# Performance work log

Hardware: AMD Instinct MI355X
Metric: run time of the kernel (lower is better)

## Reference

```python
import jax, jax.numpy as jnp
import numpy as np

N = 500000   # number of points
C = 64       # in_channels == out_channels
L = 4        # n_layers


def setup_inputs() -> dict:
    key = jax.random.key(0)
    ks = jax.random.split(key, 7)
    s = np.float32(1.0 / np.sqrt(C))  # keep activations O(1) across layers
    return {
        "features": jax.random.normal(ks[0], (N, C), jnp.float32),
        "points": jax.random.normal(ks[1], (N, 3), jnp.float32),
        "nuv": jax.random.normal(ks[2], (N, 3, 3), jnp.float32),
        "W0": jax.random.normal(ks[3], (L, C, C), jnp.float32) * s,  # linear_transform
        "b0": jnp.zeros((L, C), jnp.float32),
        "W1": jax.random.normal(ks[4], (L, C, C), jnp.float32) * s,  # linear_block[0]
        "b1": jnp.zeros((L, C), jnp.float32),
        "W2": jax.random.normal(ks[5], (L, C, C), jnp.float32) * s,  # linear_block[2]
        "b2": jnp.zeros((L, C), jnp.float32),
    }


def reference(features, points, nuv, W0, b0, W1, b1, W2, b2):
    # Faithful to the torch source: inside each DMaSIFConvBlock the dmasif_conv
    # output is overwritten by linear_transform(features), so the effective math
    # per block is: x = Linear2(relu(Linear1(Linear0(x)))).
    # points / nuv / ranges do not influence the output.
    del points, nuv

    def step(x, params):
        w0, c0, w1, c1, w2, c2 = params
        h = x @ w0 + c0                      # linear_transform
        h = jax.nn.relu(h @ w1 + c1)          # linear_block: Linear + ReLU
        h = h @ w2 + c2                      # linear_block: Linear
        return h, None

    out, _ = jax.lax.scan(step, features, (W0, b0, W1, b1, W2, b2))
    return out
```

## Files before the change

### kernel.cpp

```cpp
#include <hip/hip_runtime.h>
#include <stdint.h>

#define CH 64
#define NPTS 500000
#define NTILE (NPTS / 32)
#define NSTEP 12
#define BLK 256
#define WPB (BLK / 64)

typedef float floatx16 __attribute__((ext_vector_type(16)));
typedef __bf16 bf16x8 __attribute__((ext_vector_type(8)));

__device__ __forceinline__ unsigned pk(float odd, float even) {
    return __builtin_amdgcn_perm(__float_as_uint(odd), __float_as_uint(even), 0x07060302u);
}
__device__ __forceinline__ float hif(float x) {
    return __uint_as_float(__float_as_uint(x) & 0xffff0000u);
}

struct U16 { unsigned a, b, c, d; };
__device__ __forceinline__ bf16x8 asb4(unsigned x0, unsigned x1, unsigned x2, unsigned x3) {
    U16 t{x0, x1, x2, x3};
    return __builtin_bit_cast(bf16x8, t);
}
__device__ __forceinline__ bf16x8 asbu4(uint4 v) {
    return __builtin_bit_cast(bf16x8, v);
}

typedef __attribute__((address_space(3))) void lds_void;
typedef const __attribute__((address_space(1))) void gm_void;
__device__ __forceinline__ void gload_lds16(const void* g, void* l) {
    __builtin_amdgcn_global_load_lds((gm_void*)g, (lds_void*)l, 16, 0, 0);
}

__global__ void prep_weights(const float* __restrict__ W0,
                             const float* __restrict__ W1,
                             const float* __restrict__ W2,
                             uint4* __restrict__ wsA) {
    const int g  = blockIdx.x * blockDim.x + threadIdx.x;
    const int mp = g & 31;
    const int h  = (g >> 5) & 1;
    const int q  = (g >> 6) & 3;
    const int mt = (g >> 8) & 1;
    const int pl = (g >> 9) & 1;
    const int s  = g >> 10;
    const float* Wb = (s % 3 == 0) ? W0 : ((s % 3 == 1) ? W1 : W2);
    const float* Ws = Wb + (s / 3) * CH * CH;
    const int m   = mt * 32 + mp;
    const int col = (m & ~12) | ((m & 4) << 1) | ((m & 8) >> 1);
    unsigned o[4];
    #pragma unroll
    for (int d = 0; d < 4; ++d) {
        float e = Ws[(16 * q + 8 * h + 2 * d) * CH + col];
        float v = Ws[(16 * q + 8 * h + 2 * d + 1) * CH + col];
        if (pl) { e = e - hif(e); v = v - hif(v); }
        o[d] = pk(v, e);
    }
    wsA[g] = make_uint4(o[0], o[1], o[2], o[3]);
}

__global__ __launch_bounds__(BLK, 4) void mlp12_mfma(
    const float* __restrict__ feat,
    const uint4* __restrict__ wsA,
    const float* __restrict__ b0,
    const float* __restrict__ b1,
    const float* __restrict__ b2,
    float* __restrict__ out)
{
    __shared__ uint4 sA[2][1024];

    const int tid  = threadIdx.x;
    const int lane = tid & 63;
    const int wv   = tid >> 6;
    int wid = blockIdx.x * WPB + wv;
    if (wid > NTILE - 1) wid = NTILE - 1;
    const int n = lane & 31;
    const int h = lane >> 5;
    const size_t row = (size_t)(wid * 32 + n) * CH;

    float4 fa[4], fb[4];
    {
        const float* frow = feat + row + 8 * h;
        #pragma unroll
        for (int q = 0; q < 4; ++q) {
            fa[q] = *(const float4*)(frow + 16 * q);
            fb[q] = *(const float4*)(frow + 16 * q + 4);
        }
    }

    {
        const char* g = (const char*)wsA;
        #pragma unroll
        for (int c = 0; c < 4; ++c)
            gload_lds16(g + (wv * 4 + c) * 1024 + lane * 16,
                        (char*)&sA[0][0] + (wv * 4 + c) * 1024);
    }
    __syncthreads();

    unsigned Bhi[4][4], Blo[4][4];
    floatx16 acc0, acc1;

    #pragma unroll
    for (int s = 0; s < NSTEP; ++s) {
        const int b = s & 1;

        if (s + 1 < NSTEP) {
            const char* g = (const char*)wsA + (size_t)(s + 1) * 16384;
            #pragma unroll
            for (int c = 0; c < 4; ++c)
                gload_lds16(g + (wv * 4 + c) * 1024 + lane * 16,
                            (char*)&sA[1 - b][0] + (wv * 4 + c) * 1024);
        }

        const uint4* base = &sA[b][0];

        uint4 Acur[4], Anx[4];
        #pragma unroll
        for (int t = 0; t < 4; ++t) Acur[t] = base[(t * 4 + 0) * 64 + lane];

        if (s == 0) {
            #pragma unroll
            for (int q = 0; q < 4; ++q) {
                float e0 = fa[q].x, o0 = fa[q].y, e1 = fa[q].z, o1 = fa[q].w;
                float e2 = fb[q].x, o2 = fb[q].y, e3 = fb[q].z, o3 = fb[q].w;
                Bhi[q][0] = pk(o0, e0); Bhi[q][1] = pk(o1, e1);
                Bhi[q][2] = pk(o2, e2); Bhi[q][3] = pk(o3, e3);
                Blo[q][0] = pk(o0 - hif(o0), e0 - hif(e0));
                Blo[q][1] = pk(o1 - hif(o1), e1 - hif(e1));
                Blo[q][2] = pk(o2 - hif(o2), e2 - hif(e2));
                Blo[q][3] = pk(o3 - hif(o3), e3 - hif(e3));
            }
        } else {
            const bool relu = (s % 3 == 2);
            #pragma unroll
            for (int q = 0; q < 4; ++q) {
                const int rr = q & 1;
                #pragma unroll
                for (int d = 0; d < 4; ++d) {
                    float e, o;
                    if (q < 2) { e = acc0[8 * rr + 2 * d]; o = acc0[8 * rr + 2 * d + 1]; }
                    else       { e = acc1[8 * rr + 2 * d]; o = acc1[8 * rr + 2 * d + 1]; }
                    if (relu) { e = fmaxf(e, 0.f); o = fmaxf(o, 0.f); }
                    Bhi[q][d] = pk(o, e);
                    Blo[q][d] = pk(o - hif(o), e - hif(e));
                }
            }
        }

        {
            const float* bs = ((s % 3 == 0) ? b0 : (s % 3 == 1) ? b1 : b2) + (s / 3) * CH;
            #pragma unroll
            for (int rq = 0; rq < 4; ++rq) {
                const int off = 16 * (rq >> 1) + 8 * h + 4 * (rq & 1);
                float4 v0 = *(const float4*)(bs + off);
                float4 v1 = *(const float4*)(bs + 32 + off);
                acc0[4 * rq + 0] = v0.x; acc0[4 * rq + 1] = v0.y;
                acc0[4 * rq + 2] = v0.z; acc0[4 * rq + 3] = v0.w;
                acc1[4 * rq + 0] = v1.x; acc1[4 * rq + 1] = v1.y;
                acc1[4 * rq + 2] = v1.z; acc1[4 * rq + 3] = v1.w;
            }
        }

        #pragma unroll
        for (int q = 0; q < 4; ++q) {
            if (q < 3) {
                #pragma unroll
                for (int t = 0; t < 4; ++t) Anx[t] = base[(t * 4 + q + 1) * 64 + lane];
            }
            bf16x8 bh = asb4(Bhi[q][0], Bhi[q][1], Bhi[q][2], Bhi[q][3]);
            bf16x8 bl = asb4(Blo[q][0], Blo[q][1], Blo[q][2], Blo[q][3]);
            acc0 = __builtin_amdgcn_mfma_f32_32x32x16_bf16(asbu4(Acur[0]), bh, acc0, 0, 0, 0);
            acc1 = __builtin_amdgcn_mfma_f32_32x32x16_bf16(asbu4(Acur[1]), bh, acc1, 0, 0, 0);
            acc0 = __builtin_amdgcn_mfma_f32_32x32x16_bf16(asbu4(Acur[2]), bh, acc0, 0, 0, 0);
            acc1 = __builtin_amdgcn_mfma_f32_32x32x16_bf16(asbu4(Acur[3]), bh, acc1, 0, 0, 0);
            acc0 = __builtin_amdgcn_mfma_f32_32x32x16_bf16(asbu4(Acur[0]), bl, acc0, 0, 0, 0);
            acc1 = __builtin_amdgcn_mfma_f32_32x32x16_bf16(asbu4(Acur[1]), bl, acc1, 0, 0, 0);
            #pragma unroll
            for (int t = 0; t < 4; ++t) Acur[t] = Anx[t];
        }

        __syncthreads();
    }

    float* orow = out + row;
    #pragma unroll
    for (int rq = 0; rq < 4; ++rq) {
        float4 v0, v1;
        v0.x = acc0[4 * rq + 0]; v0.y = acc0[4 * rq + 1];
        v0.z = acc0[4 * rq + 2]; v0.w = acc0[4 * rq + 3];
        v1.x = acc1[4 * rq + 0]; v1.y = acc1[4 * rq + 1];
        v1.z = acc1[4 * rq + 2]; v1.w = acc1[4 * rq + 3];
        const int off = 16 * (rq >> 1) + 8 * h + 4 * (rq & 1);
        *(float4*)(orow + off)      = v0;
        *(float4*)(orow + 32 + off) = v1;
    }
}

extern "C" void kernel_launch(void* const* d_in, const int* in_sizes, int n_in,
                              void* d_out, int out_size, void* d_ws, size_t ws_size,
                              hipStream_t stream) {
    const float* feat = (const float*)d_in[0];
    const float* W0 = (const float*)d_in[3];
    const float* b0 = (const float*)d_in[4];
    const float* W1 = (const float*)d_in[5];
    const float* b1 = (const float*)d_in[6];
    const float* W2 = (const float*)d_in[7];
    const float* b2 = (const float*)d_in[8];
    float* out = (float*)d_out;
    uint4* wsA = (uint4*)d_ws;

    prep_weights<<<48, 256, 0, stream>>>(W0, W1, W2, wsA);

    const int grid = (NTILE + WPB - 1) / WPB;
    mlp12_mfma<<<grid, BLK, 0, stream>>>(feat, wsA, b0, b1, b2, out);
}
```

Measured before the change: 330.7 us.

## Process two 32-row tiles per wave to reuse LDS weight fragments

Each wave now computes 64 points as two independent 32-row tiles, sharing each weight fragment loaded from LDS across both tiles' MFMAs. This halves LDS weight reads and per-wave bias/setup overhead per point, and gives the MFMA pipe more independent accumulators to interleave. The 12 steps are split into two non-unrolled passes of six to bound code size. The extra accumulators and B fragments raise register pressure, so the occupancy hint drops from 4 to 3 blocks. The last wave handles its odd tile by duplicating rows.

```diff
diff --git a/kernel.cpp b/kernel.cpp
--- a/kernel.cpp
+++ b/kernel.cpp
@@ -3,7 +3,7 @@
 
 #define CH 64
 #define NPTS 500000
-#define NTILE (NPTS / 32)
+#define NW 7813
 #define NSTEP 12
 #define BLK 256
 #define WPB (BLK / 64)
@@ -32,6 +32,8 @@
 __device__ __forceinline__ void gload_lds16(const void* g, void* l) {
     __builtin_amdgcn_global_load_lds((gm_void*)g, (lds_void*)l, 16, 0, 0);
 }
+
+#define MFMA_B(A, Bv, C) __builtin_amdgcn_mfma_f32_32x32x16_bf16(asbu4(A), Bv, C, 0, 0, 0)
 
 __global__ void prep_weights(const float* __restrict__ W0,
                              const float* __restrict__ W1,
@@ -59,7 +61,7 @@
     wsA[g] = make_uint4(o[0], o[1], o[2], o[3]);
 }
 
-__global__ __launch_bounds__(BLK, 4) void mlp12_mfma(
+__global__ __launch_bounds__(BLK, 3) void mlp12_mfma(
     const float* __restrict__ feat,
     const uint4* __restrict__ wsA,
     const float* __restrict__ b0,
@@ -73,20 +75,11 @@
     const int lane = tid & 63;
     const int wv   = tid >> 6;
     int wid = blockIdx.x * WPB + wv;
-    if (wid > NTILE - 1) wid = NTILE - 1;
+    if (wid > NW - 1) wid = NW - 1;
     const int n = lane & 31;
     const int h = lane >> 5;
-    const size_t row = (size_t)(wid * 32 + n) * CH;
-
-    float4 fa[4], fb[4];
-    {
-        const float* frow = feat + row + 8 * h;
-        #pragma unroll
-        for (int q = 0; q < 4; ++q) {
-            fa[q] = *(const float4*)(frow + 16 * q);
-            fb[q] = *(const float4*)(frow + 16 * q + 4);
-        }
-    }
+    const size_t row0 = ((size_t)wid * 64 + n) * CH;
+    const size_t row1 = (wid == NW - 1) ? row0 : row0 + (size_t)32 * CH;
 
     {
         const char* g = (const char*)wsA;
@@ -95,104 +88,153 @@
             gload_lds16(g + (wv * 4 + c) * 1024 + lane * 16,
                         (char*)&sA[0][0] + (wv * 4 + c) * 1024);
     }
+
+    unsigned Bhi[2][4][4], Blo[2][4][4];
+    {
+        const float* f0 = feat + row0 + 8 * h;
+        const float* f1 = feat + row1 + 8 * h;
+        #pragma unroll
+        for (int q = 0; q < 4; ++q) {
+            float4 va = *(const float4*)(f0 + 16 * q);
+            float4 vb = *(const float4*)(f0 + 16 * q + 4);
+            Bhi[0][q][0] = pk(va.y, va.x);  Bhi[0][q][1] = pk(va.w, va.z);
+            Bhi[0][q][2] = pk(vb.y, vb.x);  Bhi[0][q][3] = pk(vb.w, vb.z);
+            Blo[0][q][0] = pk(va.y - hif(va.y), va.x - hif(va.x));
+            Blo[0][q][1] = pk(va.w - hif(va.w), va.z - hif(va.z));
+            Blo[0][q][2] = pk(vb.y - hif(vb.y), vb.x - hif(vb.x));
+            Blo[0][q][3] = pk(vb.w - hif(vb.w), vb.z - hif(vb.z));
+            float4 vc = *(const float4*)(f1 + 16 * q);
+            float4 vd = *(const float4*)(f1 + 16 * q + 4);
+            Bhi[1][q][0] = pk(vc.y, vc.x);  Bhi[1][q][1] = pk(vc.w, vc.z);
+            Bhi[1][q][2] = pk(vd.y, vd.x);  Bhi[1][q][3] = pk(vd.w, vd.z);
+            Blo[1][q][0] = pk(vc.y - hif(vc.y), vc.x - hif(vc.x));
+            Blo[1][q][1] = pk(vc.w - hif(vc.w), vc.z - hif(vc.z));
+            Blo[1][q][2] = pk(vd.y - hif(vd.y), vd.x - hif(vd.x));
+            Blo[1][q][3] = pk(vd.w - hif(vd.w), vd.z - hif(vd.z));
+        }
+    }
     __syncthreads();
 
-    unsigned Bhi[4][4], Blo[4][4];
-    floatx16 acc0, acc1;
-
-    #pragma unroll
-    for (int s = 0; s < NSTEP; ++s) {
-        const int b = s & 1;
-
-        if (s + 1 < NSTEP) {
-            const char* g = (const char*)wsA + (size_t)(s + 1) * 16384;
+    floatx16 ac00, ac01, ac10, ac11;
+
+    #pragma unroll 1
+    for (int k = 0; k < 2; ++k) {
+        const char*  gk  = (const char*)wsA + (size_t)k * 6 * 16384;
+        const float* bb0 = b0 + 2 * k * CH;
+        const float* bb1 = b1 + 2 * k * CH;
+        const float* bb2 = b2 + 2 * k * CH;
+        #pragma unroll
+        for (int j = 0; j < 6; ++j) {
+            const int s = 6 * k + j;
+            const int b = j & 1;
+
+            if (s + 1 < NSTEP) {
+                const char* g = gk + (size_t)(j + 1) * 16384;
+                #pragma unroll
+                for (int c = 0; c < 4; ++c)
+                    gload_lds16(g + (wv * 4 + c) * 1024 + lane * 16,
+                                (char*)&sA[1 - b][0] + (wv * 4 + c) * 1024);
+            }
+
+            const uint4* base = &sA[b][0];
+
+            uint4 Acur[4], Anx[4];
             #pragma unroll
-            for (int c = 0; c < 4; ++c)
-                gload_lds16(g + (wv * 4 + c) * 1024 + lane * 16,
-                            (char*)&sA[1 - b][0] + (wv * 4 + c) * 1024);
-        }
-
-        const uint4* base = &sA[b][0];
-
-        uint4 Acur[4], Anx[4];
-        #pragma unroll
-        for (int t = 0; t < 4; ++t) Acur[t] = base[(t * 4 + 0) * 64 + lane];
-
-        if (s == 0) {
+            for (int t = 0; t < 4; ++t) Acur[t] = base[(t * 4 + 0) * 64 + lane];
+
+            if (s > 0) {
+                const bool relu = (j % 3 == 2);
+                #pragma unroll
+                for (int q = 0; q < 4; ++q) {
+                    const int rr = q & 1;
+                    #pragma unroll
+                    for (int d = 0; d < 4; ++d) {
+                        float e, o;
+                        if (q < 2) { e = ac00[8*rr+2*d]; o = ac00[8*rr+2*d+1]; }
+                        else       { e = ac01[8*rr+2*d]; o = ac01[8*rr+2*d+1]; }
+                        if (relu) { e = fmaxf(e, 0.f); o = fmaxf(o, 0.f); }
+                        Bhi[0][q][d] = pk(o, e);
+                        Blo[0][q][d] = pk(o - hif(o), e - hif(e));
+                    }
+                }
+                #pragma unroll
+                for (int q = 0; q < 4; ++q) {
+                    const int rr = q & 1;
+                    #pragma unroll
+                    for (int d = 0; d < 4; ++d) {
+                        float e, o;
+                        if (q < 2) { e = ac10[8*rr+2*d]; o = ac10[8*rr+2*d+1]; }
+                        else       { e = ac11[8*rr+2*d]; o = ac11[8*rr+2*d+1]; }
+                        if (relu) { e = fmaxf(e, 0.f); o = fmaxf(o, 0.f); }
+                        Bhi[1][q][d] = pk(o, e);
+                        Blo[1][q][d] = pk(o - hif(o), e - hif(e));
+                    }
+                }
+            }
+
+            {
+                const float* bs = ((j % 3 == 0) ? bb0 : (j % 3 == 1) ? bb1 : bb2)
+                                  + (j / 3) * CH;
+                #pragma unroll
+                for (int rq = 0; rq < 4; ++rq) {
+                    const int off = 16 * (rq >> 1) + 8 * h + 4 * (rq & 1);
+                    float4 v0 = *(const float4*)(bs + off);
+                    float4 v1 = *(const float4*)(bs + 32 + off);
+                    ac00[4*rq+0] = v0.x; ac00[4*rq+1] = v0.y;
+                    ac00[4*rq+2] = v0.z; ac00[4*rq+3] = v0.w;
+                    ac10[4*rq+0] = v0.x; ac10[4*rq+1] = v0.y;
+                    ac10[4*rq+2] = v0.z; ac10[4*rq+3] = v0.w;
+                    ac01[4*rq+0] = v1.x; ac01[4*rq+1] = v1.y;
+                    ac01[4*rq+2] = v1.z; ac01[4*rq+3] = v1.w;
+                    ac11[4*rq+0] = v1.x; ac11[4*rq+1] = v1.y;
+                    ac11[4*rq+2] = v1.z; ac11[4*rq+3] = v1.w;
+                }
+            }
+
             #pragma unroll
             for (int q = 0; q < 4; ++q) {
-                float e0 = fa[q].x, o0 = fa[q].y, e1 = fa[q].z, o1 = fa[q].w;
-                float e2 = fb[q].x, o2 = fb[q].y, e3 = fb[q].z, o3 = fb[q].w;
-                Bhi[q][0] = pk(o0, e0); Bhi[q][1] = pk(o1, e1);
-                Bhi[q][2] = pk(o2, e2); Bhi[q][3] = pk(o3, e3);
-                Blo[q][0] = pk(o0 - hif(o0), e0 - hif(e0));
-                Blo[q][1] = pk(o1 - hif(o1), e1 - hif(e1));
-                Blo[q][2] = pk(o2 - hif(o2), e2 - hif(e2));
-                Blo[q][3] = pk(o3 - hif(o3), e3 - hif(e3));
-            }
-        } else {
-            const bool relu = (s % 3 == 2);
-            #pragma unroll
-            for (int q = 0; q < 4; ++q) {
-                const int rr = q & 1;
-                #pragma unroll
-                for (int d = 0; d < 4; ++d) {
-                    float e, o;
-                    if (q < 2) { e = acc0[8 * rr + 2 * d]; o = acc0[8 * rr + 2 * d + 1]; }
-                    else       { e = acc1[8 * rr + 2 * d]; o = acc1[8 * rr + 2 * d + 1]; }
-                    if (relu) { e = fmaxf(e, 0.f); o = fmaxf(o, 0.f); }
-                    Bhi[q][d] = pk(o, e);
-                    Blo[q][d] = pk(o - hif(o), e - hif(e));
-                }
-            }
+                if (q < 3) {
+                    #pragma unroll
+                    for (int t = 0; t < 4; ++t) Anx[t] = base[(t * 4 + q + 1) * 64 + lane];
+                }
+                bf16x8 b0h = asb4(Bhi[0][q][0], Bhi[0][q][1], Bhi[0][q][2], Bhi[0][q][3]);
+                bf16x8 b0l = asb4(Blo[0][q][0], Blo[0][q][1], Blo[0][q][2], Blo[0][q][3]);
+                bf16x8 b1h = asb4(Bhi[1][q][0], Bhi[1][q][1], Bhi[1][q][2], Bhi[1][q][3]);
+                bf16x8 b1l = asb4(Blo[1][q][0], Blo[1][q][1], Blo[1][q][2], Blo[1][q][3]);
+                ac00 = MFMA_B(Acur[0], b0h, ac00);
+                ac01 = MFMA_B(Acur[1], b0h, ac01);
+                ac10 = MFMA_B(Acur[0], b1h, ac10);
+                ac11 = MFMA_B(Acur[1], b1h, ac11);
+                ac00 = MFMA_B(Acur[2], b0h, ac00);
+                ac01 = MFMA_B(Acur[3], b0h, ac01);
+                ac10 = MFMA_B(Acur[2], b1h, ac10);
+                ac11 = MFMA_B(Acur[3], b1h, ac11);
+                ac00 = MFMA_B(Acur[0], b0l, ac00);
+                ac01 = MFMA_B(Acur[1], b0l, ac01);
+                ac10 = MFMA_B(Acur[0], b1l, ac10);
+                ac11 = MFMA_B(Acur[1], b1l, ac11);
+                #pragma unroll
+                for (int t = 0; t < 4; ++t) Acur[t] = Anx[t];
+            }
+
+            __syncthreads();
         }
-
-        {
-            const float* bs = ((s % 3 == 0) ? b0 : (s % 3 == 1) ? b1 : b2) + (s / 3) * CH;
-            #pragma unroll
-            for (int rq = 0; rq < 4; ++rq) {
-                const int off = 16 * (rq >> 1) + 8 * h + 4 * (rq & 1);
-                float4 v0 = *(const float4*)(bs + off);
-                float4 v1 = *(const float4*)(bs + 32 + off);
-                acc0[4 * rq + 0] = v0.x; acc0[4 * rq + 1] = v0.y;
-                acc0[4 * rq + 2] = v0.z; acc0[4 * rq + 3] = v0.w;
-                acc1[4 * rq + 0] = v1.x; acc1[4 * rq + 1] = v1.y;
-                acc1[4 * rq + 2] = v1.z; acc1[4 * rq + 3] = v1.w;
-            }
-        }
-
-        #pragma unroll
-        for (int q = 0; q < 4; ++q) {
-            if (q < 3) {
-                #pragma unroll
-                for (int t = 0; t < 4; ++t) Anx[t] = base[(t * 4 + q + 1) * 64 + lane];
-            }
-            bf16x8 bh = asb4(Bhi[q][0], Bhi[q][1], Bhi[q][2], Bhi[q][3]);
-            bf16x8 bl = asb4(Blo[q][0], Blo[q][1], Blo[q][2], Blo[q][3]);
-            acc0 = __builtin_amdgcn_mfma_f32_32x32x16_bf16(asbu4(Acur[0]), bh, acc0, 0, 0, 0);
-            acc1 = __builtin_amdgcn_mfma_f32_32x32x16_bf16(asbu4(Acur[1]), bh, acc1, 0, 0, 0);
-            acc0 = __builtin_amdgcn_mfma_f32_32x32x16_bf16(asbu4(Acur[2]), bh, acc0, 0, 0, 0);
-            acc1 = __builtin_amdgcn_mfma_f32_32x32x16_bf16(asbu4(Acur[3]), bh, acc1, 0, 0, 0);
-            acc0 = __builtin_amdgcn_mfma_f32_32x32x16_bf16(asbu4(Acur[0]), bl, acc0, 0, 0, 0);
-            acc1 = __builtin_amdgcn_mfma_f32_32x32x16_bf16(asbu4(Acur[1]), bl, acc1, 0, 0, 0);
-            #pragma unroll
-            for (int t = 0; t < 4; ++t) Acur[t] = Anx[t];
-        }
-
-        __syncthreads();
-    }
-
-    float* orow = out + row;
+    }
+
+    float* o0 = out + row0;
+    float* o1 = out + row1;
     #pragma unroll
     for (int rq = 0; rq < 4; ++rq) {
-        float4 v0, v1;
-        v0.x = acc0[4 * rq + 0]; v0.y = acc0[4 * rq + 1];
-        v0.z = acc0[4 * rq + 2]; v0.w = acc0[4 * rq + 3];
-        v1.x = acc1[4 * rq + 0]; v1.y = acc1[4 * rq + 1];
-        v1.z = acc1[4 * rq + 2]; v1.w = acc1[4 * rq + 3];
         const int off = 16 * (rq >> 1) + 8 * h + 4 * (rq & 1);
-        *(float4*)(orow + off)      = v0;
-        *(float4*)(orow + 32 + off) = v1;
+        float4 v;
+        v.x = ac00[4*rq+0]; v.y = ac00[4*rq+1]; v.z = ac00[4*rq+2]; v.w = ac00[4*rq+3];
+        *(float4*)(o0 + off) = v;
+        v.x = ac01[4*rq+0]; v.y = ac01[4*rq+1]; v.z = ac01[4*rq+2]; v.w = ac01[4*rq+3];
+        *(float4*)(o0 + 32 + off) = v;
+        v.x = ac10[4*rq+0]; v.y = ac10[4*rq+1]; v.z = ac10[4*rq+2]; v.w = ac10[4*rq+3];
+        *(float4*)(o1 + off) = v;
+        v.x = ac11[4*rq+0]; v.y = ac11[4*rq+1]; v.z = ac11[4*rq+2]; v.w = ac11[4*rq+3];
+        *(float4*)(o1 + 32 + off) = v;
     }
 }
 
@@ -211,6 +253,6 @@
 
     prep_weights<<<48, 256, 0, stream>>>(W0, W1, W2, wsA);
 
-    const int grid = (NTILE + WPB - 1) / WPB;
+    const int grid = (NW + WPB - 1) / WPB;
     mlp12_mfma<<<grid, BLK, 0, stream>>>(feat, wsA, b0, b1, b2, out);
 }
```

Result: slower. 355.2 us (+7.4%).
